# Kernel tuning notes

Measured on AMD Instinct MI355X. Metric: run time of the kernel, lower is better.

The kernel has to match this reference:

```python
import jax, jax.numpy as jnp
import numpy as np

H = 16          # num_attention_heads
DH = 64         # attention_head_size
HID = H * DH    # hidden_size = 1024
EPS = 1e-12


def _layernorm(x, gamma, beta):
    mu = jnp.mean(x, axis=-1, keepdims=True)
    var = jnp.mean(jnp.square(x - mu), axis=-1, keepdims=True)
    return (x - mu) * jax.lax.rsqrt(var + EPS) * gamma + beta


def _attention(q, k, v, mask, Wo, bo, gamma, beta):
    # q,k,v: [B,S,HID] already linearly projected
    B, Tq, _ = q.shape
    Tk = k.shape[1]
    qh = q.reshape(B, Tq, H, DH)
    kh = k.reshape(B, Tk, H, DH)
    vh = v.reshape(B, Tk, H, DH)
    scores = jnp.einsum('bqhd,bkhd->bhqk', qh, kh) / np.sqrt(DH).astype(q.dtype)
    if mask is not None:
        scores = scores + mask  # mask broadcasts [B,1,1,Tk]
    probs = jax.nn.softmax(scores, axis=-1)
    ctx = jnp.einsum('bhqk,bkhd->bqhd', probs, vh)
    proj = jnp.einsum('bqhd,hdo->bqo', ctx, Wo) + bo
    # NOTE: residual is the projected query q (faithful to the source)
    return _layernorm(q + proj, gamma, beta)


def setup_inputs() -> dict:
    key = jax.random.key(0)
    ks = jax.random.split(key, 20)
    B, T, S = 4, 1024, 1024
    s = 0.02
    inp = {
        'encoder_states': jax.random.normal(ks[0], (B, S, HID), jnp.float32),
        'decoder_inputs': jax.random.normal(ks[1], (B, T, HID), jnp.float32),
        'src_attention_mask': jnp.zeros((B, 1, 1, S), jnp.float32),
        'tgt_attention_mask': jnp.zeros((B, 1, 1, T), jnp.float32),
        'Wq': jax.random.normal(ks[2], (HID, HID), jnp.float32) * s,
        'bq': jnp.zeros((HID,), jnp.float32),
        'Wk': jax.random.normal(ks[3], (HID, HID), jnp.float32) * s,
        'bk': jnp.zeros((HID,), jnp.float32),
        'Wv': jax.random.normal(ks[4], (HID, HID), jnp.float32) * s,
        'bv': jnp.zeros((HID,), jnp.float32),
        'Wq2': jax.random.normal(ks[5], (HID, HID), jnp.float32) * s,
        'bq2': jnp.zeros((HID,), jnp.float32),
        'Wk2': jax.random.normal(ks[6], (HID, HID), jnp.float32) * s,
        'bk2': jnp.zeros((HID,), jnp.float32),
        'Wv2': jax.random.normal(ks[7], (HID, HID), jnp.float32) * s,
        'bv2': jnp.zeros((HID,), jnp.float32),
        'Wo': jax.random.normal(ks[8], (H, DH, HID), jnp.float32) * s,
        'bo': jnp.zeros((HID,), jnp.float32),
        'gamma': jnp.ones((HID,), jnp.float32),
        'beta': jnp.zeros((HID,), jnp.float32),
    }
    return inp


def reference(encoder_states, decoder_inputs, src_attention_mask, tgt_attention_mask,
              Wq, bq, Wk, bk, Wv, bv, Wq2, bq2, Wk2, bk2, Wv2, bv2,
              Wo, bo, gamma, beta):
    # self-attention over decoder inputs
    q1 = decoder_inputs @ Wq + bq
    k1 = decoder_inputs @ Wk + bk
    v1 = decoder_inputs @ Wv + bv
    self_out = _attention(q1, k1, v1, tgt_attention_mask, Wo, bo, gamma, beta)
    # cross-attention: query from self_out, key/value from encoder states
    q2 = self_out @ Wq2 + bq2
    k2 = encoder_states @ Wk2 + bk2
    v2 = encoder_states @ Wv2 + bv2
    return _attention(q2, k2, v2, src_attention_mask, Wo, bo, gamma, beta)
```

## Files before the change

kernel.cpp:

```cpp
#include <hip/hip_runtime.h>
#include <stdint.h>


typedef unsigned short u16;
typedef __bf16 bf16x8 __attribute__((ext_vector_type(8)));
typedef float f32x4 __attribute__((ext_vector_type(4)));

#define AS1 __attribute__((address_space(1)))
#define AS3 __attribute__((address_space(3)))
typedef AS3 char lds_char;
typedef AS3 unsigned short lds_u16;

#define VMCNT(n) asm volatile("s_waitcnt vmcnt(" #n ")" ::: "memory")
#define LGKM0() asm volatile("s_waitcnt lgkmcnt(0)" ::: "memory")
#define SBARRIER() asm volatile("s_barrier" ::: "memory")

__device__ __forceinline__ u16 f2bf(float f) {
  union { float f; uint32_t u; } v; v.f = f;
  uint32_t u = v.u;
  return (u16)((u + 0x7fffu + ((u >> 16) & 1u)) >> 16);
}

__device__ __forceinline__ float bf2f(u16 b) {
  union { uint32_t u; float f; } v; v.u = ((uint32_t)b) << 16;
  return v.f;
}

__device__ __forceinline__ uint32_t cvt_pk_bf16(float lo, float hi) {
  uint32_t r;
  asm("v_cvt_pk_bf16_f32 %0, %1, %2" : "=v"(r) : "v"(lo), "v"(hi));
  return r;
}

__device__ __forceinline__ void gl_lds16(const void* g, void* l) {
  __builtin_amdgcn_global_load_lds((AS1 void*)(g), (AS3 void*)(l), 16, 0, 0);
}

__device__ __forceinline__ bf16x8 dsr128(const lds_u16* p) {
  bf16x8 r;
  asm volatile("ds_read_b128 %0, %1" : "=v"(r) : "v"(p));
  return r;
}

__device__ __forceinline__ int swz(int row, int byte) {
  return row * 128 + (byte ^ ((row & 7) << 4));
}

__global__ void __launch_bounds__(256)
convert2_kernel(const float* __restrict__ in0, u16* __restrict__ out0,
                const float* __restrict__ in1, u16* __restrict__ out1) {
  const int half = blockIdx.x >> 12;
  const int i = (blockIdx.x & 4095) * 256 + threadIdx.x;
  const float* in = half ? in1 : in0;
  u16* out = half ? out1 : out0;
  float4 v = ((const float4*)in)[i];
  ushort4 o;
  o.x = f2bf(v.x); o.y = f2bf(v.y); o.z = f2bf(v.z); o.w = f2bf(v.w);
  ((ushort4*)out)[i] = o;
}

struct WP { const float* w[7]; };

__global__ void __launch_bounds__(256)
transpose_kernel(WP wp, u16* __restrict__ out) {
  __shared__ float tile[64][65];
  const float* W = wp.w[blockIdx.z];
  u16* Wt = out + (size_t)blockIdx.z * 1024 * 1024;
  const int k0 = blockIdx.y * 64, n0 = blockIdx.x * 64;
  const int t = threadIdx.x;
  const int r = t >> 4, c4 = (t & 15) * 4;
#pragma unroll
  for (int rr = 0; rr < 64; rr += 16) {
    float4 v = *(const float4*)&W[(size_t)(k0 + r + rr) * 1024 + n0 + c4];
    tile[r + rr][c4 + 0] = v.x; tile[r + rr][c4 + 1] = v.y;
    tile[r + rr][c4 + 2] = v.z; tile[r + rr][c4 + 3] = v.w;
  }
  __syncthreads();
  const int n = t >> 2, seg = (t & 3) * 16;
  union { u16 s[16]; uint4 q[2]; } u;
#pragma unroll
  for (int i = 0; i < 16; ++i) u.s[i] = f2bf(tile[seg + i][n]);
  uint4* dst = (uint4*)&Wt[(size_t)(n0 + n) * 1024 + k0 + seg];
  dst[0] = u.q[0]; dst[1] = u.q[1];
}

__global__ void __launch_bounds__(512, 4)
qkv3b_kernel(const u16* __restrict__ A0, const u16* __restrict__ A1,
             const u16* __restrict__ A2, const u16* __restrict__ Bt,
             const float* __restrict__ b0, const float* __restrict__ b1,
             const float* __restrict__ b2,
             u16* __restrict__ qb, u16* __restrict__ kb, u16* __restrict__ vt) {
  __shared__ u16 SH[36864];

  const int d = blockIdx.y * 24 + blockIdx.x;
  const int c = d & 7, ci = d >> 3;
  const int mt = ci & 15, nt = c * 3 + (ci >> 4);
  const int bm = mt * 256, bn = nt * 128;
  const int seg = nt >> 3;
  const int cs = (nt & 7) * 128;
  const u16* A = (seg == 0) ? A0 : (seg == 1) ? A1 : A2;

  const int t = threadIdx.x, wv = t >> 6, ln = t & 63;
  const int wm = (wv >> 1) * 64, wn = (wv & 1) * 64;
  const int lcol = ln & 15, g = ln >> 4;
  const int aoff = (g * 16) ^ (((lcol >> 1) & 3) << 4);

  lds_char* base = (lds_char*)&SH[0];
  const int st_srcb = (((t & 3) ^ ((t >> 3) & 3)) * 16);
  auto STAGE = [&](int buf, int k0) {
#pragma unroll
    for (int l = 0; l < 2; ++l) {
      const int row = l * 128 + (t >> 2);
      gl_lds16((const char*)A + ((size_t)(bm + row) * 1024 + k0) * 2 + st_srcb,
               (char*)base + buf * 24576 + l * 8192 + (t >> 6) * 1024);
    }
    {
      const int row = t >> 2;
      gl_lds16((const char*)Bt + ((size_t)(bn + row) * 1024 + k0) * 2 + st_srcb,
               (char*)base + buf * 24576 + 16384 + (t >> 6) * 1024);
    }
  };

  f32x4 acc[4][4] = {};

  STAGE(0, 0);
  STAGE(1, 32);
  VMCNT(3);
  __builtin_amdgcn_s_barrier();

  int cur = 0, st = 2;
  for (int kt = 0; kt < 32; ++kt) {
    lds_char* Ab = base + cur * 24576;
    lds_char* Bb = Ab + 16384;
    bf16x8 afr[4], bfr[4];
#pragma unroll
    for (int j = 0; j < 4; ++j)
      bfr[j] = dsr128((const lds_u16*)(Bb + (wn + j * 16 + lcol) * 64 + aoff));
#pragma unroll
    for (int i = 0; i < 4; ++i)
      afr[i] = dsr128((const lds_u16*)(Ab + (wm + i * 16 + lcol) * 64 + aoff));
    if (kt < 30) STAGE(st, (kt + 2) * 32);
    __builtin_amdgcn_s_barrier();
    LGKM0();
    __builtin_amdgcn_sched_barrier(0);
    __builtin_amdgcn_s_setprio(1);
#pragma unroll
    for (int i = 0; i < 4; ++i)
#pragma unroll
      for (int j = 0; j < 4; ++j)
        acc[i][j] = __builtin_amdgcn_mfma_f32_16x16x32_bf16(afr[i], bfr[j], acc[i][j], 0, 0, 0);
    __builtin_amdgcn_s_setprio(0);
    if (kt < 30)       { VMCNT(3); }
    else if (kt == 30) { VMCNT(0); }
    __builtin_amdgcn_s_barrier();
    cur = (cur == 2) ? 0 : cur + 1;
    st  = (st == 2)  ? 0 : st + 1;
  }

  const float* bias = (seg == 0) ? b0 : (seg == 1) ? b1 : b2;

  if (seg == 2) {
#pragma unroll
    for (int j = 0; j < 4; ++j) {
      const int col_l = wn + j * 16 + lcol;
      const float bc = bias[cs + col_l];
#pragma unroll
      for (int i = 0; i < 4; ++i) {
        const int m4 = wm + i * 16 + g * 4;
        ushort4 o;
        o.x = f2bf(acc[i][j][0] + bc); o.y = f2bf(acc[i][j][1] + bc);
        o.z = f2bf(acc[i][j][2] + bc); o.w = f2bf(acc[i][j][3] + bc);
        *(ushort4*)((char*)SH + col_l * 512 + ((m4 * 2) ^ ((col_l & 7) << 4))) = o;
      }
    }
  } else {
#pragma unroll
    for (int j = 0; j < 4; ++j) {
      const int col_l = wn + j * 16 + lcol;
      const float bc = bias[cs + col_l];
#pragma unroll
      for (int i = 0; i < 4; ++i) {
        const int m0 = wm + i * 16 + g * 4;
#pragma unroll
        for (int r = 0; r < 4; ++r)
          SH[(m0 + r) * 128 + (col_l ^ (((m0 + r) & 7) << 3))] = f2bf(acc[i][j][r] + bc);
      }
    }
  }
  __builtin_amdgcn_s_barrier();

  if (seg == 2) {
    const int C = t >> 2, q = t & 3;
    const int col = cs + C;
    const int h = col >> 6, dd = col & 63;
    u16* gp = vt + ((size_t)((bm >> 10) * 16 + h) * 64 + dd) * 1024 + (bm & 1023) + q * 64;
#pragma unroll
    for (int cix = 0; cix < 8; ++cix) {
      uint4 v = *(uint4*)((char*)SH + C * 512 + ((q * 128 + cix * 16) ^ ((C & 7) << 4)));
      *(uint4*)(gp + cix * 8) = v;
    }
  } else {
    const int R = t >> 1, hb = t & 1;
    u16* outp = (seg == 0) ? qb : kb;
    u16* gp = outp + (size_t)(bm + R) * 1024 + cs + hb * 64;
#pragma unroll
    for (int cix = 0; cix < 8; ++cix) {
      uint4 v = *(uint4*)((char*)SH + R * 256 + ((hb * 128 + cix * 16) ^ ((R & 7) << 4)));
      *(uint4*)(gp + cix * 8) = v;
    }
  }
}

__global__ void __launch_bounds__(256)
gemm_proj(const u16* __restrict__ A, const u16* __restrict__ Bt,
          const float* __restrict__ bias, const u16* __restrict__ resid,
          float* __restrict__ outf) {
  __shared__ u16 Alds[3][8192];
  __shared__ u16 Blds[3][8192];
  const int d = blockIdx.y * 8 + blockIdx.x;
  const int c = d & 7, ci = d >> 3;
  const int mt = (c & 3) * 8 + (ci & 7);
  const int nt = (c >> 2) * 4 + (ci >> 3);
  const int bm = mt * 128, bn = nt * 128;
  const int t = threadIdx.x, wv = t >> 6, ln = t & 63;
  const int wm = (wv >> 1) * 64, wn = (wv & 1) * 64;
  const int lcol = ln & 15, g = ln >> 4, lr4 = g * 4;
  const int xr = (lcol & 7) << 4;
  const int aoff0 = (g * 16) ^ xr;
  const int aoff1 = (64 + g * 16) ^ xr;

  f32x4 acc[4][4] = {};

  const int st_srcb = (((t & 7) ^ ((t >> 3) & 7)) * 16);
  auto STAGE = [&](int buf, int k0) {
#pragma unroll
    for (int l = 0; l < 4; ++l) {
      const int row = l * 32 + (t >> 3);
      gl_lds16((const char*)A + ((size_t)(bm + row) * 1024 + k0) * 2 + st_srcb,
               (char*)&Alds[buf][0] + l * 4096 + (t >> 6) * 1024);
      gl_lds16((const char*)Bt + ((size_t)(bn + row) * 1024 + k0) * 2 + st_srcb,
               (char*)&Blds[buf][0] + l * 4096 + (t >> 6) * 1024);
    }
  };

  STAGE(0, 0);
  STAGE(1, 64);
  VMCNT(8);
  __builtin_amdgcn_s_barrier();

  int cur = 0, st = 2;
  for (int it = 0; it < 16; ++it) {
    lds_char* Ab = (lds_char*)&Alds[cur][0];
    lds_char* Bb = (lds_char*)&Blds[cur][0];
    bf16x8 a0[4], b0v[4], a1[4], b1v[4];
#pragma unroll
    for (int i = 0; i < 4; ++i) {
      a0[i]  = dsr128((const lds_u16*)(Ab + (wm + i * 16 + lcol) * 128 + aoff0));
      b0v[i] = dsr128((const lds_u16*)(Bb + (wn + i * 16 + lcol) * 128 + aoff0));
    }
#pragma unroll
    for (int i = 0; i < 4; ++i) {
      a1[i]  = dsr128((const lds_u16*)(Ab + (wm + i * 16 + lcol) * 128 + aoff1));
      b1v[i] = dsr128((const lds_u16*)(Bb + (wn + i * 16 + lcol) * 128 + aoff1));
    }
    if (it < 14) STAGE(st, (it + 2) * 64);
    __builtin_amdgcn_s_barrier();
    LGKM0();
    __builtin_amdgcn_sched_barrier(0);
    __builtin_amdgcn_s_setprio(1);
#pragma unroll
    for (int i = 0; i < 4; ++i)
#pragma unroll
      for (int j = 0; j < 4; ++j)
        acc[i][j] = __builtin_amdgcn_mfma_f32_16x16x32_bf16(a0[i], b0v[j], acc[i][j], 0, 0, 0);
#pragma unroll
    for (int i = 0; i < 4; ++i)
#pragma unroll
      for (int j = 0; j < 4; ++j)
        acc[i][j] = __builtin_amdgcn_mfma_f32_16x16x32_bf16(a1[i], b1v[j], acc[i][j], 0, 0, 0);
    __builtin_amdgcn_s_setprio(0);
    if (it < 14)       { VMCNT(8); }
    else if (it == 14) { VMCNT(0); }
    __builtin_amdgcn_s_barrier();
    cur = (cur == 2) ? 0 : cur + 1;
    st  = (st == 2)  ? 0 : st + 1;
  }

#pragma unroll
  for (int j = 0; j < 4; ++j) {
    const int col = bn + wn + j * 16 + lcol;
    const float bc = bias[col];
#pragma unroll
    for (int i = 0; i < 4; ++i) {
      const int row0 = bm + wm + i * 16 + lr4;
#pragma unroll
      for (int r = 0; r < 4; ++r) {
        const size_t idx = (size_t)(row0 + r) * 1024 + col;
        outf[idx] = acc[i][j][r] + bc + bf2f(resid[idx]);
      }
    }
  }
}

__global__ void __launch_bounds__(512)
attn_kernel(const u16* __restrict__ Q, const u16* __restrict__ Kb,
            const u16* __restrict__ Vt, const float* __restrict__ mask,
            u16* __restrict__ ctx) {
  __shared__ u16 Klds[2][64 * 64];
  __shared__ u16 Vlds[2][64 * 64];
  __shared__ u16 Plds[8][16 * 64];

  const int fid = blockIdx.x;
  const int xcd = fid & 7, idx = fid >> 3;
  const int bh = xcd * 8 + (idx >> 3);
  const int b = bh >> 4, h = bh & 15;
  const int q0 = (idx & 7) * 128;

  const int t = threadIdx.x, wv = t >> 6, ln = t & 63;
  const int lcol = ln & 15, g = ln >> 4;
  const int lk8 = g * 8, c0 = g * 16;

  const int qrow = q0 + wv * 16 + lcol;
  const u16* qptr = Q + ((size_t)(b * 1024 + qrow) * 1024 + h * 64);
  bf16x8 qa[2];
  qa[0] = *(const bf16x8*)(qptr + lk8);
  qa[1] = *(const bf16x8*)(qptr + 32 + lk8);

  const float* mrow = mask + b * 1024;
  char* pbase = (char*)&Plds[wv][0];

  f32x4 accO[4] = {};
  float m_r = -1e30f, l_r = 0.f;

  const int st_row = t >> 3;
  const int st_srcb = (((t & 7) ^ ((t >> 3) & 7)) * 16);
  auto STAGE = [&](int buf, int s0) {
    gl_lds16((const char*)Kb + ((size_t)((b * 1024 + s0 + st_row) * 1024 + h * 64)) * 2 + st_srcb,
             (char*)Klds[buf] + wv * 1024);
    gl_lds16((const char*)Vt + ((size_t)(((b * 16 + h) * 64 + st_row) * 1024 + s0)) * 2 + st_srcb,
             (char*)Vlds[buf] + wv * 1024);
  };

  auto TILE = [&](int buf, const float4* mk) {
    f32x4 accST[4] = {};
    __builtin_amdgcn_s_setprio(1);
#pragma unroll
    for (int ks = 0; ks < 2; ++ks)
#pragma unroll
      for (int sb = 0; sb < 4; ++sb) {
        bf16x8 kb = *(const bf16x8*)((const char*)Klds[buf] + swz(sb * 16 + lcol, ks * 64 + c0));
        accST[sb] = __builtin_amdgcn_mfma_f32_16x16x32_bf16(kb, qa[ks], accST[sb], 0, 0, 0);
      }
    __builtin_amdgcn_s_setprio(0);

    float sv[4][4];
#pragma unroll
    for (int sb = 0; sb < 4; ++sb) {
      sv[sb][0] = accST[sb][0] * 0.125f + mk[sb].x;
      sv[sb][1] = accST[sb][1] * 0.125f + mk[sb].y;
      sv[sb][2] = accST[sb][2] * 0.125f + mk[sb].z;
      sv[sb][3] = accST[sb][3] * 0.125f + mk[sb].w;
    }
    float mt = sv[0][0];
#pragma unroll
    for (int sb = 0; sb < 4; ++sb)
#pragma unroll
      for (int r = 0; r < 4; ++r) mt = fmaxf(mt, sv[sb][r]);
    mt = fmaxf(mt, __shfl_xor(mt, 16));
    mt = fmaxf(mt, __shfl_xor(mt, 32));

    const bool nr = __all(mt <= m_r + 8.0f) != 0;
    float alpha = 1.0f;
    if (!nr) {
      const float mn2 = fmaxf(m_r, mt);
      alpha = __expf(m_r - mn2);
      m_r = mn2;
    }
    float rs = 0.f;
#pragma unroll
    for (int sb = 0; sb < 4; ++sb)
#pragma unroll
      for (int r = 0; r < 4; ++r) {
        const float pp = __expf(sv[sb][r] - m_r);
        sv[sb][r] = pp;
        rs += pp;
      }
    rs += __shfl_xor(rs, 16);
    rs += __shfl_xor(rs, 32);
    l_r = nr ? (l_r + rs) : (l_r * alpha + rs);

#pragma unroll
    for (int sb = 0; sb < 4; ++sb) {
      uint2 dd;
      dd.x = cvt_pk_bf16(sv[sb][0], sv[sb][1]);
      dd.y = cvt_pk_bf16(sv[sb][2], sv[sb][3]);
      *(uint2*)(pbase + swz(lcol, sb * 32 + g * 8)) = dd;
    }

    if (!nr) {
#pragma unroll
      for (int df = 0; df < 4; ++df)
#pragma unroll
        for (int r = 0; r < 4; ++r) accO[df][r] *= alpha;
    }
    __builtin_amdgcn_s_setprio(1);
#pragma unroll
    for (int ks = 0; ks < 2; ++ks) {
      bf16x8 pb = *(const bf16x8*)(pbase + swz(lcol, ks * 64 + c0));
#pragma unroll
      for (int df = 0; df < 4; ++df) {
        bf16x8 va = *(const bf16x8*)((const char*)Vlds[buf] + swz(df * 16 + lcol, ks * 64 + c0));
        accO[df] = __builtin_amdgcn_mfma_f32_16x16x32_bf16(va, pb, accO[df], 0, 0, 0);
      }
    }
    __builtin_amdgcn_s_setprio(0);
  };

  STAGE(0, 0);
  float4 mk_cur[4];
#pragma unroll
  for (int sb = 0; sb < 4; ++sb)
    mk_cur[sb] = *(const float4*)&mrow[sb * 16 + g * 4];

  int cur = 0;
  for (int ti = 0; ti < 15; ++ti) {
    const int s1 = ti * 64 + 64;
    STAGE(cur ^ 1, s1);
    float4 mk_nxt[4];
#pragma unroll
    for (int sb = 0; sb < 4; ++sb)
      mk_nxt[sb] = *(const float4*)&mrow[s1 + sb * 16 + g * 4];
    VMCNT(10);
    SBARRIER();
    TILE(cur, mk_cur);
    SBARRIER();
#pragma unroll
    for (int sb = 0; sb < 4; ++sb) mk_cur[sb] = mk_nxt[sb];
    cur ^= 1;
  }
  VMCNT(4);
  SBARRIER();
  TILE(cur, mk_cur);

  const float inv = 1.0f / l_r;
  u16* cp = ctx + ((size_t)(b * 1024 + qrow) * 1024 + h * 64);
#pragma unroll
  for (int df = 0; df < 4; ++df) {
    ushort4 o;
    o.x = f2bf(accO[df][0] * inv); o.y = f2bf(accO[df][1] * inv);
    o.z = f2bf(accO[df][2] * inv); o.w = f2bf(accO[df][3] * inv);
    *(ushort4*)(cp + df * 16 + g * 4) = o;
  }
}

template <int OUTF>
__global__ void __launch_bounds__(256)
ln_kernel(const float* __restrict__ x, const float* __restrict__ gamma,
          const float* __restrict__ beta, float* __restrict__ outf,
          u16* __restrict__ outb) {
  const int row = blockIdx.x, t = threadIdx.x;
  const float* xr = x + (size_t)row * 1024;
  float4 v = *(const float4*)&xr[t * 4];
  float s = v.x + v.y + v.z + v.w;
  float q = v.x * v.x + v.y * v.y + v.z * v.z + v.w * v.w;
#pragma unroll
  for (int off = 1; off < 64; off <<= 1) {
    s += __shfl_xor(s, off);
    q += __shfl_xor(q, off);
  }
  __shared__ float ws[4], wq[4];
  if ((t & 63) == 0) { ws[t >> 6] = s; wq[t >> 6] = q; }
  __syncthreads();
  s = ws[0] + ws[1] + ws[2] + ws[3];
  q = wq[0] + wq[1] + wq[2] + wq[3];
  const float mu = s * (1.0f / 1024.0f);
  float var = q * (1.0f / 1024.0f) - mu * mu;
  var = fmaxf(var, 0.0f);
  const float rstd = rsqrtf(var + 1e-12f);
  float4 g = *(const float4*)&gamma[t * 4];
  float4 be = *(const float4*)&beta[t * 4];
  float y0 = (v.x - mu) * rstd * g.x + be.x;
  float y1 = (v.y - mu) * rstd * g.y + be.y;
  float y2 = (v.z - mu) * rstd * g.z + be.z;
  float y3 = (v.w - mu) * rstd * g.w + be.w;
  if constexpr (OUTF) {
    float4 o; o.x = y0; o.y = y1; o.z = y2; o.w = y3;
    *(float4*)&outf[(size_t)row * 1024 + t * 4] = o;
  } else {
    ushort4 o; o.x = f2bf(y0); o.y = f2bf(y1); o.z = f2bf(y2); o.w = f2bf(y3);
    *(ushort4*)&outb[(size_t)row * 1024 + t * 4] = o;
  }
}

extern "C" void kernel_launch(void* const* d_in, const int* in_sizes, int n_in,
                              void* d_out, int out_size, void* d_ws, size_t ws_size,
                              hipStream_t stream) {
  const float* enc = (const float*)d_in[0];
  const float* dec = (const float*)d_in[1];
  const float* src_mask = (const float*)d_in[2];
  const float* tgt_mask = (const float*)d_in[3];
  const float* Wq  = (const float*)d_in[4];  const float* bq  = (const float*)d_in[5];
  const float* Wk  = (const float*)d_in[6];  const float* bk  = (const float*)d_in[7];
  const float* Wv  = (const float*)d_in[8];  const float* bv  = (const float*)d_in[9];
  const float* Wq2 = (const float*)d_in[10]; const float* bq2 = (const float*)d_in[11];
  const float* Wk2 = (const float*)d_in[12]; const float* bk2 = (const float*)d_in[13];
  const float* Wv2 = (const float*)d_in[14]; const float* bv2 = (const float*)d_in[15];
  const float* Wo  = (const float*)d_in[16]; const float* bo  = (const float*)d_in[17];
  const float* gamma = (const float*)d_in[18]; const float* beta = (const float*)d_in[19];
  float* out = (float*)d_out;

  char* p = (char*)d_ws;
  const size_t ABF = (size_t)4096 * 1024 * 2;
  const size_t AF  = (size_t)4096 * 1024 * 4;
  const size_t WBF = (size_t)1024 * 1024 * 2;
  u16* decbf = (u16*)p; p += ABF;
  u16* encbf = (u16*)p; p += ABF;
  u16* wt    = (u16*)p; p += 7 * WBF;
  u16* qbf   = (u16*)p; p += ABF;
  u16* kbf   = (u16*)p; p += ABF;
  u16* vtb   = (u16*)p; p += ABF;
  u16* ctxb  = (u16*)p; p += ABF;
  float* tmpf = (float*)p; p += AF;
  u16* sobf  = decbf;

  u16* WoT  = wt + 6 * 1048576;

  dim3 b256(256);
  convert2_kernel<<<8192, b256, 0, stream>>>(dec, decbf, enc, encbf);
  WP wp;
  wp.w[0] = Wq; wp.w[1] = Wk; wp.w[2] = Wv; wp.w[3] = Wq2;
  wp.w[4] = Wk2; wp.w[5] = Wv2; wp.w[6] = Wo;
  transpose_kernel<<<dim3(16, 16, 7), b256, 0, stream>>>(wp, wt);

  qkv3b_kernel<<<dim3(24, 16), 512, 0, stream>>>(
      decbf, decbf, decbf, wt, bq, bk, bv, qbf, kbf, vtb);
  attn_kernel<<<512, 512, 0, stream>>>(qbf, kbf, vtb, tgt_mask, ctxb);
  gemm_proj<<<dim3(8, 32), b256, 0, stream>>>(ctxb, WoT, bo, qbf, tmpf);
  ln_kernel<0><<<4096, b256, 0, stream>>>(tmpf, gamma, beta, nullptr, sobf);
  qkv3b_kernel<<<dim3(24, 16), 512, 0, stream>>>(
      sobf, encbf, encbf, wt + 3 * 1048576, bq2, bk2, bv2, qbf, kbf, vtb);
  attn_kernel<<<512, 512, 0, stream>>>(qbf, kbf, vtb, src_mask, ctxb);
  gemm_proj<<<dim3(8, 32), b256, 0, stream>>>(ctxb, WoT, bo, qbf, tmpf);
  ln_kernel<1><<<4096, b256, 0, stream>>>(tmpf, gamma, beta, out, nullptr);
}
```

Before: 211.7 us.

## Shrink QKV GEMM tiles to 128x128 and load B fragments directly to registers

The fused QKV projection kernel moves from 512-thread 256x128 tiles to 256-thread 128x128 tiles, doubling the grid to 768 blocks. The B operand is no longer staged through LDS: each wave reads its weight fragments from global memory straight into registers, one k-step ahead. Only A is triple-buffered in LDS, which cuts shared memory use, and the block-to-tile mapping is regrouped per XCD. The aim is better occupancy and fewer LDS round trips, at the cost of redundant global B loads across waves and less reuse per tile.

```diff
diff --git a/kernel.cpp b/kernel.cpp
--- a/kernel.cpp
+++ b/kernel.cpp
@@ -84,18 +84,19 @@
   dst[0] = u.q[0]; dst[1] = u.q[1];
 }
 
-__global__ void __launch_bounds__(512, 4)
-qkv3b_kernel(const u16* __restrict__ A0, const u16* __restrict__ A1,
+__global__ void __launch_bounds__(256, 3)
+qkv4g_kernel(const u16* __restrict__ A0, const u16* __restrict__ A1,
              const u16* __restrict__ A2, const u16* __restrict__ Bt,
              const float* __restrict__ b0, const float* __restrict__ b1,
              const float* __restrict__ b2,
              u16* __restrict__ qb, u16* __restrict__ kb, u16* __restrict__ vt) {
-  __shared__ u16 SH[36864];
+  __shared__ u16 SH[16384];
 
   const int d = blockIdx.y * 24 + blockIdx.x;
-  const int c = d & 7, ci = d >> 3;
-  const int mt = ci & 15, nt = c * 3 + (ci >> 4);
-  const int bm = mt * 256, bn = nt * 128;
+  const int xcd = d & 7, ci = d >> 3;
+  const int mt = (xcd & 3) * 8 + (ci & 7);
+  const int nt = (xcd >> 2) * 12 + (ci >> 3);
+  const int bm = mt * 128, bn = nt * 128;
   const int seg = nt >> 3;
   const int cs = (nt & 7) * 128;
   const u16* A = (seg == 0) ? A0 : (seg == 1) ? A1 : A2;
@@ -106,41 +107,46 @@
   const int aoff = (g * 16) ^ (((lcol >> 1) & 3) << 4);
 
   lds_char* base = (lds_char*)&SH[0];
+
   const int st_srcb = (((t & 3) ^ ((t >> 3) & 3)) * 16);
-  auto STAGE = [&](int buf, int k0) {
+  auto stageA = [&](int buf, int k0) {
 #pragma unroll
     for (int l = 0; l < 2; ++l) {
-      const int row = l * 128 + (t >> 2);
+      const int row = l * 64 + (t >> 2);
       gl_lds16((const char*)A + ((size_t)(bm + row) * 1024 + k0) * 2 + st_srcb,
-               (char*)base + buf * 24576 + l * 8192 + (t >> 6) * 1024);
-    }
-    {
-      const int row = t >> 2;
-      gl_lds16((const char*)Bt + ((size_t)(bn + row) * 1024 + k0) * 2 + st_srcb,
-               (char*)base + buf * 24576 + 16384 + (t >> 6) * 1024);
+               (char*)base + buf * 8192 + l * 4096 + wv * 1024);
     }
   };
 
+  const u16* Bbase = Bt + (size_t)(bn + wn + lcol) * 1024 + g * 8;
+
   f32x4 acc[4][4] = {};
-
-  STAGE(0, 0);
-  STAGE(1, 32);
-  VMCNT(3);
+  bf16x8 Bcur[4], Bnxt[4];
+
+  stageA(0, 0);
+#pragma unroll
+  for (int j = 0; j < 4; ++j)
+    Bcur[j] = *(const bf16x8*)(Bbase + (size_t)j * 16 * 1024);
+  stageA(1, 32);
+  VMCNT(2);
   __builtin_amdgcn_s_barrier();
 
   int cur = 0, st = 2;
   for (int kt = 0; kt < 32; ++kt) {
-    lds_char* Ab = base + cur * 24576;
-    lds_char* Bb = Ab + 16384;
-    bf16x8 afr[4], bfr[4];
-#pragma unroll
-    for (int j = 0; j < 4; ++j)
-      bfr[j] = dsr128((const lds_u16*)(Bb + (wn + j * 16 + lcol) * 64 + aoff));
+    lds_char* Ab = base + cur * 8192;
+    bf16x8 afr[4];
 #pragma unroll
     for (int i = 0; i < 4; ++i)
       afr[i] = dsr128((const lds_u16*)(Ab + (wm + i * 16 + lcol) * 64 + aoff));
-    if (kt < 30) STAGE(st, (kt + 2) * 32);
+    if (kt < 31) {
+      const int k1 = (kt + 1) * 32;
+#pragma unroll
+      for (int j = 0; j < 4; ++j)
+        Bnxt[j] = *(const bf16x8*)(Bbase + (size_t)j * 16 * 1024 + k1);
+    }
+    if (kt < 30) stageA(st, (kt + 2) * 32);
     __builtin_amdgcn_s_barrier();
+    if (kt == 31) VMCNT(0);
     LGKM0();
     __builtin_amdgcn_sched_barrier(0);
     __builtin_amdgcn_s_setprio(1);
@@ -148,11 +154,13 @@
     for (int i = 0; i < 4; ++i)
 #pragma unroll
       for (int j = 0; j < 4; ++j)
-        acc[i][j] = __builtin_amdgcn_mfma_f32_16x16x32_bf16(afr[i], bfr[j], acc[i][j], 0, 0, 0);
+        acc[i][j] = __builtin_amdgcn_mfma_f32_16x16x32_bf16(afr[i], Bcur[j], acc[i][j], 0, 0, 0);
     __builtin_amdgcn_s_setprio(0);
-    if (kt < 30)       { VMCNT(3); }
-    else if (kt == 30) { VMCNT(0); }
+    if (kt < 30)       { VMCNT(2); }
+    else if (kt == 30) { VMCNT(4); }
     __builtin_amdgcn_s_barrier();
+#pragma unroll
+    for (int j = 0; j < 4; ++j) Bcur[j] = Bnxt[j];
     cur = (cur == 2) ? 0 : cur + 1;
     st  = (st == 2)  ? 0 : st + 1;
   }
@@ -170,7 +178,7 @@
         ushort4 o;
         o.x = f2bf(acc[i][j][0] + bc); o.y = f2bf(acc[i][j][1] + bc);
         o.z = f2bf(acc[i][j][2] + bc); o.w = f2bf(acc[i][j][3] + bc);
-        *(ushort4*)((char*)SH + col_l * 512 + ((m4 * 2) ^ ((col_l & 7) << 4))) = o;
+        *(ushort4*)((char*)SH + col_l * 256 + ((m4 * 2) ^ ((col_l & 7) << 4))) = o;
       }
     }
   } else {
@@ -190,13 +198,13 @@
   __builtin_amdgcn_s_barrier();
 
   if (seg == 2) {
-    const int C = t >> 2, q = t & 3;
+    const int C = t >> 1, hb = t & 1;
     const int col = cs + C;
     const int h = col >> 6, dd = col & 63;
-    u16* gp = vt + ((size_t)((bm >> 10) * 16 + h) * 64 + dd) * 1024 + (bm & 1023) + q * 64;
+    u16* gp = vt + ((size_t)((bm >> 10) * 16 + h) * 64 + dd) * 1024 + (bm & 1023) + hb * 64;
 #pragma unroll
     for (int cix = 0; cix < 8; ++cix) {
-      uint4 v = *(uint4*)((char*)SH + C * 512 + ((q * 128 + cix * 16) ^ ((C & 7) << 4)));
+      uint4 v = *(uint4*)((char*)SH + C * 256 + ((hb * 128 + cix * 16) ^ ((C & 7) << 4)));
       *(uint4*)(gp + cix * 8) = v;
     }
   } else {
@@ -532,12 +540,12 @@
   wp.w[4] = Wk2; wp.w[5] = Wv2; wp.w[6] = Wo;
   transpose_kernel<<<dim3(16, 16, 7), b256, 0, stream>>>(wp, wt);
 
-  qkv3b_kernel<<<dim3(24, 16), 512, 0, stream>>>(
+  qkv4g_kernel<<<dim3(24, 32), b256, 0, stream>>>(
       decbf, decbf, decbf, wt, bq, bk, bv, qbf, kbf, vtb);
   attn_kernel<<<512, 512, 0, stream>>>(qbf, kbf, vtb, tgt_mask, ctxb);
   gemm_proj<<<dim3(8, 32), b256, 0, stream>>>(ctxb, WoT, bo, qbf, tmpf);
   ln_kernel<0><<<4096, b256, 0, stream>>>(tmpf, gamma, beta, nullptr, sobf);
-  qkv3b_kernel<<<dim3(24, 16), 512, 0, stream>>>(
+  qkv4g_kernel<<<dim3(24, 32), b256, 0, stream>>>(
       sobf, encbf, encbf, wt + 3 * 1048576, bq2, bk2, bv2, qbf, kbf, vtb);
   attn_kernel<<<512, 512, 0, stream>>>(qbf, kbf, vtb, src_mask, ctxb);
   gemm_proj<<<dim3(8, 32), b256, 0, stream>>>(ctxb, WoT, bo, qbf, tmpf);
```

After: 251.2 us. +18.7%, slower.
